# Kernel optimization log

Hardware: AMD Instinct MI355X
Metric: run time of the kernel (lower is better)

## Reference

```python
import jax, jax.numpy as jnp
import numpy as np


def setup_inputs() -> dict:
    key = jax.random.key(0)
    ks = jax.random.split(key, 7)
    T, B, I, H = 512, 64, 512, 512
    s_ih = 1.0 / np.sqrt(H)
    return {
        "input": jax.random.normal(ks[0], (T, B, I), dtype=jnp.float32),
        "h0": jax.random.normal(ks[1], (B, H), dtype=jnp.float32),
        "c0": jax.random.normal(ks[2], (B, H), dtype=jnp.float32),
        "W_ih": jax.random.normal(ks[3], (4 * H, I), dtype=jnp.float32) * s_ih,
        "W_hh": jax.random.normal(ks[4], (4 * H, H), dtype=jnp.float32) * s_ih,
        "b_ih": jax.random.normal(ks[5], (4 * H,), dtype=jnp.float32) * s_ih,
        "b_hh": jax.random.normal(ks[6], (4 * H,), dtype=jnp.float32) * s_ih,
    }


def _lstm_scan(input, h0, c0, W_ih, W_hh, b_ih, b_hh):
    H = h0.shape[-1]
    # Precompute input-side gate projections for all timesteps: [T, B, 4H]
    x_gates = jnp.einsum("tbi,gi->tbg", input, W_ih) + b_ih + b_hh

    def step(carry, xg):
        h, c = carry
        gates = xg + h @ W_hh.T  # [B, 4H]
        i, f, g, o = jnp.split(gates, 4, axis=-1)  # PyTorch i,f,g,o order
        i = jax.nn.sigmoid(i)
        f = jax.nn.sigmoid(f)
        g = jnp.tanh(g)
        o = jax.nn.sigmoid(o)
        c = f * c + i * g
        h = o * jnp.tanh(c)
        return (h, c), h

    (hT, cT), outputs = jax.lax.scan(step, (h0, c0), x_gates)
    return outputs, hT, cT


def reference(input, h0, c0, W_ih, W_hh, b_ih, b_hh):
    # Returns (stacked outputs [T,B,H], final h, final c)
    return _lstm_scan(input, h0, c0, W_ih, W_hh, b_ih, b_hh)
```

## Files before the change

kernel.cpp:

```cpp
#include <hip/hip_runtime.h>
#include <hip/hip_bf16.h>


typedef __attribute__((ext_vector_type(8))) short short8;
typedef __attribute__((ext_vector_type(4))) float f32x4;

#define T_STEPS 512
#define BATCH   64
#define HID     512
#define GATES   2048
#define BH      (BATCH * HID)
#define NBLOCKS 32
#define WCHUNKS (4 * 16 * 64)
#define RING    3

__device__ __forceinline__ unsigned short f2bfu(float f) {
    union { __hip_bfloat16 h; unsigned short s; } u;
    u.h = __float2bfloat16(f);
    return u.s;
}
__device__ __forceinline__ float sigmoidf_fast(float x) {
    return 1.0f / (1.0f + __expf(-x));
}
__device__ __forceinline__ float tanhf_fast(float x) {
    return 2.0f / (1.0f + __expf(-2.0f * x)) - 1.0f;
}
__device__ __forceinline__ short8 sysload16(const unsigned short* p) {
    short8 r;
    asm volatile("global_load_dwordx4 %0, %1, off sc0 sc1"
                 : "=v"(r) : "v"(p) : "memory");
    return r;
}

__global__ __launch_bounds__(256) void prep(
    const float* __restrict__ h0,
    const float* __restrict__ W_ih, const float* __restrict__ W_hh,
    const float* __restrict__ b_ih, const float* __restrict__ b_hh,
    unsigned short* __restrict__ WihF, unsigned short* __restrict__ WhhF,
    unsigned short* __restrict__ hbuf0, float* __restrict__ bias,
    int* __restrict__ hflag)
{
    const int tid = blockIdx.x * 256 + threadIdx.x;
    {
        const int which = (tid >= 131072);
        const int t2   = tid & 131071;
        const int lane = t2 & 63;
        const int kb   = (t2 >> 6) & 15;
        const int g    = (t2 >> 10) & 3;
        const int jt   = t2 >> 12;
        const float* W = which ? W_hh : W_ih;
        unsigned short* F = which ? WhhF : WihF;
        const int row = g * HID + jt * 16 + (lane & 15);
        const int k   = kb * 32 + (lane >> 4) * 8;
        const float* src = W + (size_t)row * HID + k;
        unsigned short* dst = F + ((((size_t)jt * 4 + g) * 16 + kb) * 64 + lane) * 8;
#pragma unroll
        for (int j = 0; j < 8; ++j) dst[j] = f2bfu(src[j]);
    }
    if (tid < GATES)   bias[tid]  = b_ih[tid] + b_hh[tid];
    if (tid < BH)      hbuf0[tid] = f2bfu(h0[tid]);
    if (tid < T_STEPS * NBLOCKS) hflag[tid] = 0;
}

__global__ __launch_bounds__(512, 2) void lstm_persistent(
    const float* __restrict__ input,
    const float* __restrict__ c0,
    const unsigned short* __restrict__ WihF,
    const unsigned short* __restrict__ WhhF,
    const float* __restrict__ bias,
    unsigned short* __restrict__ hbuf,
    int* __restrict__ hflag,
    float* __restrict__ out)
{
    __shared__ f32x4 ring[RING][4][256];
    __shared__ int xg_ready[RING][4];
    __shared__ int cons[4];
    __shared__ int arr2[2];
    __shared__ int mirror;

    const int tid  = threadIdx.x;
    const int lane = tid & 63;
    const int w    = tid >> 6;
    const int bt   = w & 3;
    const int jt   = blockIdx.x;
    const int quad = lane >> 4;
    const int lr   = lane & 15;

    if (tid < RING * 4)              (&xg_ready[0][0])[tid] = 0;
    else if (tid < RING * 4 + 4)     cons[tid - RING * 4] = 0;
    else if (tid < RING * 4 + 6)     arr2[tid - RING * 4 - 4] = 0;
    else if (tid == RING * 4 + 6)    mirror = 0;
    __syncthreads();

    const int brow  = bt * 16 + lr;
    const int jbase = jt * 16 + quad * 4;

    if (w >= 4) {
        float bs[4][4];
#pragma unroll
        for (int g = 0; g < 4; ++g)
#pragma unroll
            for (int r = 0; r < 4; ++r)
                bs[g][r] = bias[g * HID + jbase + r];
        const unsigned short* wih_lane =
            WihF + (size_t)jt * WCHUNKS * 8 + (size_t)lane * 8;

        for (int t = 0; t < T_STEPS; ++t) {
            const int s = t % RING;
            if (t >= RING) {
                while (__hip_atomic_load(&cons[bt], __ATOMIC_ACQUIRE,
                                         __HIP_MEMORY_SCOPE_WORKGROUP) < t - (RING - 1))
                    __builtin_amdgcn_s_sleep(2);
            }
            f32x4 acc[4];
#pragma unroll
            for (int g = 0; g < 4; ++g)
                acc[g] = (f32x4){bs[g][0], bs[g][1], bs[g][2], bs[g][3]};
            const float* xp = input + ((size_t)t * BATCH + brow) * HID + quad * 8;
#pragma unroll
            for (int kb = 0; kb < 16; ++kb) {
                const f32x4 f0 = *reinterpret_cast<const f32x4*>(xp + kb * 32);
                const f32x4 f1 = *reinterpret_cast<const f32x4*>(xp + kb * 32 + 4);
                union { __hip_bfloat162 b2[4]; short8 s8; } bu;
                bu.b2[0] = __float22bfloat162_rn(make_float2(f0.x, f0.y));
                bu.b2[1] = __float22bfloat162_rn(make_float2(f0.z, f0.w));
                bu.b2[2] = __float22bfloat162_rn(make_float2(f1.x, f1.y));
                bu.b2[3] = __float22bfloat162_rn(make_float2(f1.z, f1.w));
#pragma unroll
                for (int g = 0; g < 4; ++g) {
                    short8 afrag = *reinterpret_cast<const short8*>(
                        wih_lane + ((size_t)(g * 16 + kb) * 64) * 8);
                    acc[g] = __builtin_amdgcn_mfma_f32_16x16x32_bf16(
                        afrag, bu.s8, acc[g], 0, 0, 0);
                }
            }
#pragma unroll
            for (int g = 0; g < 4; ++g)
                ring[s][g][bt * 64 + lane] = acc[g];
            __hip_atomic_store(&xg_ready[s][bt], t + 1, __ATOMIC_RELEASE,
                               __HIP_MEMORY_SCOPE_WORKGROUP);
        }
        return;
    }

    __builtin_amdgcn_s_setprio(1);

    f32x4 c = *reinterpret_cast<const f32x4*>(c0 + (size_t)brow * HID + jbase);
    const unsigned short* whh_lane =
        WhhF + (size_t)jt * WCHUNKS * 8 + (size_t)lane * 8;
    float hlast[4];

    for (int t = 0; t < T_STEPS; ++t) {
        const int s = t % RING;

        while (__hip_atomic_load(&xg_ready[s][bt], __ATOMIC_ACQUIRE,
                                 __HIP_MEMORY_SCOPE_WORKGROUP) < t + 1)
            __builtin_amdgcn_s_sleep(1);
        f32x4 xg[4];
#pragma unroll
        for (int g = 0; g < 4; ++g) xg[g] = ring[s][g][bt * 64 + lane];

        if (t > 0) {
            if (w == 0) {
                int* hf = hflag + (size_t)(t - 1) * NBLOCKS;
                for (;;) {
                    int f = (lane < NBLOCKS)
                        ? __hip_atomic_load(&hf[lane], __ATOMIC_RELAXED,
                                            __HIP_MEMORY_SCOPE_SYSTEM)
                        : 1;
                    if (__all(f != 0)) break;
                    __builtin_amdgcn_s_sleep(1);
                }
                __hip_atomic_store(&mirror, t, __ATOMIC_RELEASE,
                                   __HIP_MEMORY_SCOPE_WORKGROUP);
            } else {
                while (__hip_atomic_load(&mirror, __ATOMIC_ACQUIRE,
                                         __HIP_MEMORY_SCOPE_WORKGROUP) < t)
                    __builtin_amdgcn_s_sleep(1);
            }
            __atomic_signal_fence(__ATOMIC_ACQ_REL);
            __builtin_amdgcn_sched_barrier(0);
        }

        const unsigned short* hp =
            hbuf + (size_t)(t & 1) * BH + (size_t)brow * HID + quad * 8;
        short8 hreg[16];
#pragma unroll
        for (int kb = 0; kb < 16; ++kb) hreg[kb] = sysload16(hp + kb * 32);
        asm volatile("s_waitcnt vmcnt(0)" ::: "memory");
        __builtin_amdgcn_sched_barrier(0);

        f32x4 acc[4];
#pragma unroll
        for (int g = 0; g < 4; ++g) acc[g] = (f32x4){0.f, 0.f, 0.f, 0.f};
#pragma unroll
        for (int kb = 0; kb < 16; ++kb) {
#pragma unroll
            for (int g = 0; g < 4; ++g) {
                short8 afrag = *reinterpret_cast<const short8*>(
                    whh_lane + ((size_t)(g * 16 + kb) * 64) * 8);
                acc[g] = __builtin_amdgcn_mfma_f32_16x16x32_bf16(
                    afrag, hreg[kb], acc[g], 0, 0, 0);
            }
        }

        unsigned long long hpack = 0;
        f32x4 outv;
#pragma unroll
        for (int r = 0; r < 4; ++r) {
            const float i_ = sigmoidf_fast(acc[0][r] + xg[0][r]);
            const float f_ = sigmoidf_fast(acc[1][r] + xg[1][r]);
            const float g_ = tanhf_fast(acc[2][r] + xg[2][r]);
            const float o_ = sigmoidf_fast(acc[3][r] + xg[3][r]);
            const float cr = f_ * c[r] + i_ * g_;
            c[r] = cr;
            const float h = o_ * tanhf_fast(cr);
            hlast[r] = h;
            outv[r] = h;
            hpack |= (unsigned long long)f2bfu(h) << (16 * r);
        }

        __hip_atomic_store(reinterpret_cast<unsigned long long*>(
                               hbuf + (size_t)((t + 1) & 1) * BH +
                               (size_t)brow * HID + jbase),
                           hpack, __ATOMIC_RELAXED, __HIP_MEMORY_SCOPE_SYSTEM);
        __threadfence_block();
        __hip_atomic_store(&cons[bt], t + 1, __ATOMIC_RELEASE,
                           __HIP_MEMORY_SCOPE_WORKGROUP);
        if (lane == 0) {
            int old = atomicAdd(&arr2[t & 1], 1);
            if (old == 3) {
                arr2[t & 1] = 0;
                __hip_atomic_store(&hflag[(size_t)t * NBLOCKS + jt], 1,
                                   __ATOMIC_RELAXED, __HIP_MEMORY_SCOPE_SYSTEM);
            }
        }

        __builtin_nontemporal_store(
            outv, reinterpret_cast<f32x4*>(
                      out + ((size_t)t * BATCH + brow) * HID + jbase));
    }

    float* hT = out + (size_t)T_STEPS * BH;
    float* cT = hT + BH;
    f32x4 hv4;
#pragma unroll
    for (int r = 0; r < 4; ++r) hv4[r] = hlast[r];
    *reinterpret_cast<f32x4*>(hT + (size_t)brow * HID + jbase) = hv4;
    *reinterpret_cast<f32x4*>(cT + (size_t)brow * HID + jbase) = c;
}

extern "C" void kernel_launch(void* const* d_in, const int* in_sizes, int n_in,
                              void* d_out, int out_size, void* d_ws, size_t ws_size,
                              hipStream_t stream) {
    const float* input = (const float*)d_in[0];
    const float* h0    = (const float*)d_in[1];
    const float* c0    = (const float*)d_in[2];
    const float* W_ih  = (const float*)d_in[3];
    const float* W_hh  = (const float*)d_in[4];
    const float* b_ih  = (const float*)d_in[5];
    const float* b_hh  = (const float*)d_in[6];
    float* out = (float*)d_out;

    char* ws = (char*)d_ws;
    unsigned short* WihF = (unsigned short*)ws;
    unsigned short* WhhF = WihF + (size_t)GATES * HID;
    unsigned short* hbuf = WhhF + (size_t)GATES * HID;
    float* bias = (float*)(hbuf + 2 * BH);
    int* hflag = (int*)(bias + GATES);

    prep<<<1024, 256, 0, stream>>>(h0, W_ih, W_hh, b_ih, b_hh,
                                   WihF, WhhF, hbuf, bias, hflag);

    lstm_persistent<<<NBLOCKS, 512, 0, stream>>>(
        input, c0, WihF, WhhF, bias, hbuf, hflag, out);
}
```

Measured before the change: 6.530 ms.

## Keep LSTM weights in registers and LDS, prefetch next-step input gates

```diff
diff --git a/kernel.cpp b/kernel.cpp
--- a/kernel.cpp
+++ b/kernel.cpp
@@ -72,6 +72,7 @@
     int* __restrict__ hflag,
     float* __restrict__ out)
 {
+    __shared__ unsigned short WhhL[WCHUNKS * 8];
     __shared__ f32x4 ring[RING][4][256];
     __shared__ int xg_ready[RING][4];
     __shared__ int cons[4];
@@ -90,6 +91,13 @@
     else if (tid < RING * 4 + 4)     cons[tid - RING * 4] = 0;
     else if (tid < RING * 4 + 6)     arr2[tid - RING * 4 - 4] = 0;
     else if (tid == RING * 4 + 6)    mirror = 0;
+
+    {
+        const short8* src = reinterpret_cast<const short8*>(
+            WhhF + (size_t)jt * WCHUNKS * 8);
+        short8* dst = reinterpret_cast<short8*>(WhhL);
+        for (int idx = tid; idx < WCHUNKS; idx += 512) dst[idx] = src[idx];
+    }
     __syncthreads();
 
     const int brow  = bt * 16 + lr;
@@ -104,6 +112,14 @@
                 bs[g][r] = bias[g * HID + jbase + r];
         const unsigned short* wih_lane =
             WihF + (size_t)jt * WCHUNKS * 8 + (size_t)lane * 8;
+
+        short8 wih_reg[2][16];
+#pragma unroll
+        for (int g = 0; g < 2; ++g)
+#pragma unroll
+            for (int kb = 0; kb < 16; ++kb)
+                wih_reg[g][kb] = *reinterpret_cast<const short8*>(
+                    wih_lane + ((size_t)(g * 16 + kb) * 64) * 8);
 
         for (int t = 0; t < T_STEPS; ++t) {
             const int s = t % RING;
@@ -127,7 +143,11 @@
                 bu.b2[2] = __float22bfloat162_rn(make_float2(f1.x, f1.y));
                 bu.b2[3] = __float22bfloat162_rn(make_float2(f1.z, f1.w));
 #pragma unroll
-                for (int g = 0; g < 4; ++g) {
+                for (int g = 0; g < 2; ++g)
+                    acc[g] = __builtin_amdgcn_mfma_f32_16x16x32_bf16(
+                        wih_reg[g][kb], bu.s8, acc[g], 0, 0, 0);
+#pragma unroll
+                for (int g = 2; g < 4; ++g) {
                     short8 afrag = *reinterpret_cast<const short8*>(
                         wih_lane + ((size_t)(g * 16 + kb) * 64) * 8);
                     acc[g] = __builtin_amdgcn_mfma_f32_16x16x32_bf16(
@@ -146,20 +166,28 @@
     __builtin_amdgcn_s_setprio(1);
 
     f32x4 c = *reinterpret_cast<const f32x4*>(c0 + (size_t)brow * HID + jbase);
-    const unsigned short* whh_lane =
-        WhhF + (size_t)jt * WCHUNKS * 8 + (size_t)lane * 8;
     float hlast[4];
 
+    short8 whh_reg[2][16];
+#pragma unroll
+    for (int g = 0; g < 2; ++g)
+#pragma unroll
+        for (int kb = 0; kb < 16; ++kb)
+            whh_reg[g][kb] =
+                reinterpret_cast<const short8*>(WhhL)[(g * 16 + kb) * 64 + lane];
+
+    f32x4 xg[4];
+    {
+        while (__hip_atomic_load(&xg_ready[0][bt], __ATOMIC_ACQUIRE,
+                                 __HIP_MEMORY_SCOPE_WORKGROUP) < 1)
+            __builtin_amdgcn_s_sleep(1);
+#pragma unroll
+        for (int g = 0; g < 4; ++g) xg[g] = ring[0][g][bt * 64 + lane];
+        __hip_atomic_store(&cons[bt], 1, __ATOMIC_RELEASE,
+                           __HIP_MEMORY_SCOPE_WORKGROUP);
+    }
+
     for (int t = 0; t < T_STEPS; ++t) {
-        const int s = t % RING;
-
-        while (__hip_atomic_load(&xg_ready[s][bt], __ATOMIC_ACQUIRE,
-                                 __HIP_MEMORY_SCOPE_WORKGROUP) < t + 1)
-            __builtin_amdgcn_s_sleep(1);
-        f32x4 xg[4];
-#pragma unroll
-        for (int g = 0; g < 4; ++g) xg[g] = ring[s][g][bt * 64 + lane];
-
         if (t > 0) {
             if (w == 0) {
                 int* hf = hflag + (size_t)(t - 1) * NBLOCKS;
@@ -196,9 +224,13 @@
 #pragma unroll
         for (int kb = 0; kb < 16; ++kb) {
 #pragma unroll
-            for (int g = 0; g < 4; ++g) {
-                short8 afrag = *reinterpret_cast<const short8*>(
-                    whh_lane + ((size_t)(g * 16 + kb) * 64) * 8);
+            for (int g = 0; g < 2; ++g)
+                acc[g] = __builtin_amdgcn_mfma_f32_16x16x32_bf16(
+                    whh_reg[g][kb], hreg[kb], acc[g], 0, 0, 0);
+#pragma unroll
+            for (int g = 2; g < 4; ++g) {
+                short8 afrag =
+                    reinterpret_cast<const short8*>(WhhL)[(g * 16 + kb) * 64 + lane];
                 acc[g] = __builtin_amdgcn_mfma_f32_16x16x32_bf16(
                     afrag, hreg[kb], acc[g], 0, 0, 0);
             }
@@ -224,9 +256,10 @@
                                hbuf + (size_t)((t + 1) & 1) * BH +
                                (size_t)brow * HID + jbase),
                            hpack, __ATOMIC_RELAXED, __HIP_MEMORY_SCOPE_SYSTEM);
+        __builtin_nontemporal_store(
+            outv, reinterpret_cast<f32x4*>(
+                      out + ((size_t)t * BATCH + brow) * HID + jbase));
         __threadfence_block();
-        __hip_atomic_store(&cons[bt], t + 1, __ATOMIC_RELEASE,
-                           __HIP_MEMORY_SCOPE_WORKGROUP);
         if (lane == 0) {
             int old = atomicAdd(&arr2[t & 1], 1);
             if (old == 3) {
@@ -236,9 +269,16 @@
             }
         }
 
-        __builtin_nontemporal_store(
-            outv, reinterpret_cast<f32x4*>(
-                      out + ((size_t)t * BATCH + brow) * HID + jbase));
+        if (t + 1 < T_STEPS) {
+            const int sn = (t + 1) % RING;
+            while (__hip_atomic_load(&xg_ready[sn][bt], __ATOMIC_ACQUIRE,
+                                     __HIP_MEMORY_SCOPE_WORKGROUP) < t + 2)
+                __builtin_amdgcn_s_sleep(1);
+#pragma unroll
+            for (int g = 0; g < 4; ++g) xg[g] = ring[sn][g][bt * 64 + lane];
+            __hip_atomic_store(&cons[bt], t + 2, __ATOMIC_RELEASE,
+                               __HIP_MEMORY_SCOPE_WORKGROUP);
+        }
     }
 
     float* hT = out + (size_t)T_STEPS * BH;
```

Result: faster. 5.725 ms (-12.3%).
